# Kernel tuning notes

Measured on AMD Instinct MI355X. Metric: run time of the kernel, lower is better.

## Reference

```python
import jax, jax.numpy as jnp
import numpy as np

B, T, C = 4, 2048, 1024
H, D = 16, 64  # num_heads, head_size; H*D == C


def setup_inputs() -> dict:
    key = jax.random.key(0)
    k1, k2, k3 = jax.random.split(key, 3)
    x = jax.random.normal(k1, (B, T, C), dtype=jnp.float32)
    w_qkv = jax.random.normal(k2, (C, 3 * C), dtype=jnp.float32) * (C ** -0.5)
    w_out = jax.random.normal(k3, (C, C), dtype=jnp.float32) * (C ** -0.5)
    b_out = jnp.zeros((C,), dtype=jnp.float32)
    return {"x": x, "w_qkv": w_qkv, "w_out": w_out, "b_out": b_out}


def reference(x, w_qkv, w_out, b_out):
    Bb, Tt, Cc = x.shape
    qkv = x @ w_qkv                        # [B,T,3C]
    q, k, v = jnp.split(qkv, 3, axis=2)
    # [B,T,C] -> [B,H,T,D]
    q = q.reshape(Bb, Tt, H, D).transpose(0, 2, 1, 3)
    k = k.reshape(Bb, Tt, H, D).transpose(0, 2, 1, 3)
    v = v.reshape(Bb, Tt, H, D).transpose(0, 2, 1, 3)
    scores = jnp.einsum('bhqd,bhkd->bhqk', q, k) * (D ** -0.5)
    causal = jnp.tril(jnp.ones((Tt, Tt), dtype=bool))
    scores = jnp.where(causal, scores, -jnp.inf)
    attn = jax.nn.softmax(scores, axis=-1)  # dropout is identity in eval mode
    out = jnp.einsum('bhqk,bhkd->bhqd', attn, v)
    out = out.transpose(0, 2, 1, 3).reshape(Bb, Tt, Cc)
    return out @ w_out + b_out
```

## Files before the change

### kernel.cpp

```cpp
#include <hip/hip_runtime.h>

typedef __bf16 bf16;
typedef __bf16 bf16x4 __attribute__((ext_vector_type(4)));
typedef __bf16 bf16x8 __attribute__((ext_vector_type(8)));
typedef float  f32x4  __attribute__((ext_vector_type(4)));

#define MFMA16(A_, B_, C_) __builtin_amdgcn_mfma_f32_16x16x32_bf16((A_), (B_), (C_), 0, 0, 0)

#define BB 4
#define TT 2048
#define CC 1024
#define HH 16
#define DD 64
#define MM (BB * TT)
#define N_QKV (3 * CC)
#define LDSS 68
#define BSTRIDE 36
#define QSCALE 0.125f

static __device__ __forceinline__ void store_lds8(bf16* p, bf16x8 v) {
  bf16x4 lo, hi;
#pragma unroll
  for (int i = 0; i < 4; i++) { lo[i] = v[i]; hi[i] = v[i + 4]; }
  *(bf16x4*)p = lo;
  *(bf16x4*)(p + 4) = hi;
}

static __device__ __forceinline__ bf16x8 load_lds8(const bf16* p) {
  bf16x4 lo = *(const bf16x4*)p;
  bf16x4 hi = *(const bf16x4*)(p + 4);
  bf16x8 v;
#pragma unroll
  for (int i = 0; i < 4; i++) { v[i] = lo[i]; v[i + 4] = hi[i]; }
  return v;
}

__global__ __launch_bounds__(256) void sniff_k(const unsigned short* __restrict__ u,
                                               int* __restrict__ flag) {
  __shared__ int s;
  if (threadIdx.x == 0) s = 0;
  __syncthreads();
  int c = 0;
  for (int i = threadIdx.x; i < 65536; i += 256)
    if ((u[i] & 0x7F80u) == 0x7F80u) c = 1;
  if (c) atomicOr(&s, 1);
  __syncthreads();
  if (threadIdx.x == 0) *flag = s;
}

__global__ __launch_bounds__(256) void cvt_k(const void* __restrict__ in,
                                             bf16* __restrict__ out,
                                             const int* __restrict__ flag) {
  const int fl = *flag;
  const size_t i = ((size_t)blockIdx.x * 256 + threadIdx.x) * 8;
  if (fl) {
    f32x4 a = *(const f32x4*)((const float*)in + i);
    f32x4 b = *(const f32x4*)((const float*)in + i + 4);
    bf16x8 o;
#pragma unroll
    for (int j = 0; j < 4; j++) { o[j] = (bf16)a[j]; o[4 + j] = (bf16)b[j]; }
    *(bf16x8*)(out + i) = o;
  } else {
    *(bf16x8*)(out + i) = *(const bf16x8*)((const bf16*)in + i);
  }
}

__global__ __launch_bounds__(256) void transpose_k(const void* __restrict__ in,
                                                   bf16* __restrict__ out,
                                                   int R, int C,
                                                   const int* __restrict__ flag) {
  __shared__ bf16 tile[32][33];
  const int fl = *flag;
  const int c0 = blockIdx.x * 32, r0 = blockIdx.y * 32;
  const int tx = threadIdx.x & 31, ty = threadIdx.x >> 5;
#pragma unroll
  for (int i = ty; i < 32; i += 8) {
    const size_t idx = (size_t)(r0 + i) * C + c0 + tx;
    tile[i][tx] = fl ? (bf16)((const float*)in)[idx] : ((const bf16*)in)[idx];
  }
  __syncthreads();
#pragma unroll
  for (int i = ty; i < 32; i += 8)
    out[(size_t)(c0 + i) * R + r0 + tx] = tile[tx][i];
}

template <int EPI, bool AF>
__global__ __launch_bounds__(256) void gemm_bt(const void* __restrict__ Av,
                                               const bf16* __restrict__ Bt,
                                               const void* __restrict__ biasv,
                                               void* __restrict__ Cv,
                                               const int* __restrict__ flag,
                                               size_t aoff, size_t coff,
                                               int M, int N, int K,
                                               int lda, int ldc) {
  const int fl = *flag;
  const bool af32 = AF && (fl != 0);
  __shared__ __align__(16) bf16 sA[128 * 32];
  __shared__ __align__(16) bf16 sB[128 * 32];
  const int tid = threadIdx.x;
  const int lane = tid & 63, wave = tid >> 6;
  const int quad = lane >> 4, l15 = lane & 15;
  const int wr = wave >> 1, wc = wave & 1;
  const int m0 = blockIdx.x * 128, n0 = blockIdx.y * 128;
  const int srow = tid >> 2;
  const int scol = (tid & 3) * 8;

  f32x4 acc[4][4];
#pragma unroll
  for (int i = 0; i < 4; i++)
#pragma unroll
    for (int j = 0; j < 4; j++) {
      f32x4 z = {0.f, 0.f, 0.f, 0.f};
      acc[i][j] = z;
    }

  const size_t abase0 = aoff + (size_t)(m0 + srow) * lda + scol;
  const size_t abase1 = abase0 + (size_t)64 * lda;
  const bf16* Bg0 = Bt + (size_t)(n0 + srow) * K + scol;
  const bf16* Bg1 = Bg0 + (size_t)64 * K;

  for (int k0 = 0; k0 < K; k0 += 32) {
    bf16x8 a0, a1;
    if (af32) {
      const float* Af = (const float*)Av;
      f32x4 p00 = *(const f32x4*)(Af + abase0 + k0);
      f32x4 p01 = *(const f32x4*)(Af + abase0 + k0 + 4);
      f32x4 p10 = *(const f32x4*)(Af + abase1 + k0);
      f32x4 p11 = *(const f32x4*)(Af + abase1 + k0 + 4);
#pragma unroll
      for (int i = 0; i < 4; i++) {
        a0[i] = (bf16)p00[i]; a0[i + 4] = (bf16)p01[i];
        a1[i] = (bf16)p10[i]; a1[i + 4] = (bf16)p11[i];
      }
    } else {
      const bf16* Ab = (const bf16*)Av;
      a0 = *(const bf16x8*)(Ab + abase0 + k0);
      a1 = *(const bf16x8*)(Ab + abase1 + k0);
    }
    bf16x8 b0 = *(const bf16x8*)(Bg0 + k0);
    bf16x8 b1 = *(const bf16x8*)(Bg1 + k0);
    __syncthreads();
    *(bf16x8*)(sA + srow * 32 + scol) = a0;
    *(bf16x8*)(sA + (64 + srow) * 32 + scol) = a1;
    *(bf16x8*)(sB + srow * 32 + scol) = b0;
    *(bf16x8*)(sB + (64 + srow) * 32 + scol) = b1;
    __syncthreads();

    bf16x8 af[4], bfr[4];
#pragma unroll
    for (int mi = 0; mi < 4; mi++)
      af[mi] = *(const bf16x8*)(sA + (wr * 64 + mi * 16 + l15) * 32 + quad * 8);
#pragma unroll
    for (int ni = 0; ni < 4; ni++)
      bfr[ni] = *(const bf16x8*)(sB + (wc * 64 + ni * 16 + l15) * 32 + quad * 8);
#pragma unroll
    for (int mi = 0; mi < 4; mi++)
#pragma unroll
      for (int ni = 0; ni < 4; ni++)
        acc[mi][ni] = MFMA16(af[mi], bfr[ni], acc[mi][ni]);
  }

#pragma unroll
  for (int mi = 0; mi < 4; mi++) {
#pragma unroll
    for (int r = 0; r < 4; r++) {
      const int m = m0 + wr * 64 + mi * 16 + quad * 4 + r;
#pragma unroll
      for (int ni = 0; ni < 4; ni++) {
        const int n = n0 + wc * 64 + ni * 16 + l15;
        float v = acc[mi][ni][r];
        const size_t idx = coff + (size_t)m * ldc + n;
        if (EPI == 1) {
          v += fl ? ((const float*)biasv)[n] : (float)((const bf16*)biasv)[n];
          if (fl) ((float*)Cv)[idx] = v;
          else    ((bf16*)Cv)[idx] = (bf16)v;
        } else {
          ((bf16*)Cv)[idx] = (bf16)v;
        }
      }
    }
  }
}

template <int EPI, bool AF, bool WF>
__global__ __launch_bounds__(256) void gemm_nt(const void* __restrict__ Av,
                                               const void* __restrict__ Wv,
                                               const void* __restrict__ biasv,
                                               void* __restrict__ Cv,
                                               const int* __restrict__ flag,
                                               size_t aoff, size_t coff,
                                               int M, int N, int K,
                                               int lda, int ldc) {
  const int fl = *flag;
  const bool af32 = AF && (fl != 0);
  const bool wf32 = WF && (fl != 0);
  __shared__ __align__(16) bf16 sA[128 * 32];
  __shared__ __align__(16) bf16 sB[128 * BSTRIDE];
  const int tid = threadIdx.x;
  const int lane = tid & 63, wave = tid >> 6;
  const int quad = lane >> 4, l15 = lane & 15;
  const int wr = wave >> 1, wc = wave & 1;
  const int m0 = blockIdx.x * 128, n0 = blockIdx.y * 128;
  const int arow = tid >> 2, acol = (tid & 3) * 8;
  const int wk = tid >> 3, wn = (tid & 7) * 16;

  f32x4 acc[4][4];
#pragma unroll
  for (int i = 0; i < 4; i++)
#pragma unroll
    for (int j = 0; j < 4; j++) {
      f32x4 z = {0.f, 0.f, 0.f, 0.f};
      acc[i][j] = z;
    }

  const size_t abase0 = aoff + (size_t)(m0 + arow) * lda + acol;
  const size_t abase1 = abase0 + (size_t)64 * lda;

  for (int k0 = 0; k0 < K; k0 += 32) {
    bf16x8 a0, a1;
    if (af32) {
      const float* Af = (const float*)Av;
      f32x4 p00 = *(const f32x4*)(Af + abase0 + k0);
      f32x4 p01 = *(const f32x4*)(Af + abase0 + k0 + 4);
      f32x4 p10 = *(const f32x4*)(Af + abase1 + k0);
      f32x4 p11 = *(const f32x4*)(Af + abase1 + k0 + 4);
#pragma unroll
      for (int i = 0; i < 4; i++) {
        a0[i] = (bf16)p00[i]; a0[i + 4] = (bf16)p01[i];
        a1[i] = (bf16)p10[i]; a1[i + 4] = (bf16)p11[i];
      }
    } else {
      const bf16* Ab = (const bf16*)Av;
      a0 = *(const bf16x8*)(Ab + abase0 + k0);
      a1 = *(const bf16x8*)(Ab + abase1 + k0);
    }
    bf16 wreg[16];
    const size_t wbase = (size_t)(k0 + wk) * N + n0 + wn;
    if (wf32) {
      const float* Wf = (const float*)Wv;
      f32x4 q0 = *(const f32x4*)(Wf + wbase);
      f32x4 q1 = *(const f32x4*)(Wf + wbase + 4);
      f32x4 q2 = *(const f32x4*)(Wf + wbase + 8);
      f32x4 q3 = *(const f32x4*)(Wf + wbase + 12);
#pragma unroll
      for (int i = 0; i < 4; i++) {
        wreg[i] = (bf16)q0[i];      wreg[4 + i] = (bf16)q1[i];
        wreg[8 + i] = (bf16)q2[i];  wreg[12 + i] = (bf16)q3[i];
      }
    } else {
      const bf16* Wb = (const bf16*)Wv;
      bf16x8 w0 = *(const bf16x8*)(Wb + wbase);
      bf16x8 w1 = *(const bf16x8*)(Wb + wbase + 8);
#pragma unroll
      for (int i = 0; i < 8; i++) { wreg[i] = w0[i]; wreg[8 + i] = w1[i]; }
    }
    __syncthreads();
    *(bf16x8*)(sA + arow * 32 + acol) = a0;
    *(bf16x8*)(sA + (64 + arow) * 32 + acol) = a1;
#pragma unroll
    for (int i = 0; i < 16; i++)
      sB[(wn + i) * BSTRIDE + wk] = wreg[i];
    __syncthreads();

    bf16x8 af[4], bfr[4];
#pragma unroll
    for (int mi = 0; mi < 4; mi++)
      af[mi] = *(const bf16x8*)(sA + (wr * 64 + mi * 16 + l15) * 32 + quad * 8);
#pragma unroll
    for (int ni = 0; ni < 4; ni++)
      bfr[ni] = load_lds8(sB + (wc * 64 + ni * 16 + l15) * BSTRIDE + quad * 8);
#pragma unroll
    for (int mi = 0; mi < 4; mi++)
#pragma unroll
      for (int ni = 0; ni < 4; ni++)
        acc[mi][ni] = MFMA16(af[mi], bfr[ni], acc[mi][ni]);
  }

#pragma unroll
  for (int mi = 0; mi < 4; mi++) {
#pragma unroll
    for (int r = 0; r < 4; r++) {
      const int m = m0 + wr * 64 + mi * 16 + quad * 4 + r;
#pragma unroll
      for (int ni = 0; ni < 4; ni++) {
        const int n = n0 + wc * 64 + ni * 16 + l15;
        float v = acc[mi][ni][r];
        const size_t idx = coff + (size_t)m * ldc + n;
        if (EPI == 1) {
          v += fl ? ((const float*)biasv)[n] : (float)((const bf16*)biasv)[n];
          if (fl) ((float*)Cv)[idx] = v;
          else    ((bf16*)Cv)[idx] = (bf16)v;
        } else {
          ((bf16*)Cv)[idx] = (bf16)v;
        }
      }
    }
  }
}

__global__ __launch_bounds__(256) void attn_k(bf16* __restrict__ qkv) {
  __shared__ __align__(16) bf16 sQ[128 * LDSS];
  __shared__ __align__(16) bf16 sK[64 * LDSS];
  __shared__ __align__(16) bf16 sVt[64 * LDSS];

  const int tid = threadIdx.x;
  const int lane = tid & 63, wave = tid >> 6;
  const int quad = lane >> 4, l15 = lane & 15;
  const int bh = blockIdx.y;
  bf16* base = qkv + (size_t)(bh >> 4) * TT * N_QKV + (bh & 15) * DD;
  const bf16* Qp = base;
  const bf16* Kp = base + CC;
  const bf16* Vp = base + 2 * CC;

  const int krow = tid >> 2;
  const int kcol = (tid & 3) * 16;
  const int vkey = tid & 31;
  const int vcol = (tid >> 5) * 8;

  bf16x8 ones;
  {
    const bf16 o = (l15 == 0) ? (bf16)1.0f : (bf16)0.0f;
#pragma unroll
    for (int i = 0; i < 8; i++) ones[i] = o;
  }

  for (int pass = 0; pass < 2; pass++) {
    const int qt = pass ? (15 - (int)blockIdx.x) : (int)blockIdx.x;
    const int q0 = qt * 128;
    __syncthreads();

#pragma unroll
    for (int p = 0; p < 2; p++) {
      const int r = p * 64 + krow;
      const bf16* src = Qp + (size_t)(q0 + r) * N_QKV + kcol;
      bf16x8 v0 = *(const bf16x8*)src;
      bf16x8 v1 = *(const bf16x8*)(src + 8);
#pragma unroll
      for (int i = 0; i < 8; i++) {
        v0[i] = (bf16)((float)v0[i] * QSCALE);
        v1[i] = (bf16)((float)v1[i] * QSCALE);
      }
      store_lds8(sQ + r * LDSS + kcol, v0);
      store_lds8(sQ + r * LDSS + kcol + 8, v1);
    }

    bf16x8 kr0, kr1, vr0, vr1;
    {
      const bf16* kp = Kp + (size_t)krow * N_QKV + kcol;
      kr0 = *(const bf16x8*)kp;
      kr1 = *(const bf16x8*)(kp + 8);
      vr0 = *(const bf16x8*)(Vp + (size_t)vkey * N_QKV + vcol);
      vr1 = *(const bf16x8*)(Vp + (size_t)(32 + vkey) * N_QKV + vcol);
    }
    __syncthreads();

    bf16x8 aq[2][2];
#pragma unroll
    for (int mi = 0; mi < 2; mi++) {
      const bf16* qp = sQ + (size_t)(wave * 32 + mi * 16 + l15) * LDSS + quad * 8;
      aq[mi][0] = load_lds8(qp);
      aq[mi][1] = load_lds8(qp + 32);
    }

    f32x4 Oacc[2][4];
    f32x4 lacc[2];
#pragma unroll
    for (int mi = 0; mi < 2; mi++) {
      f32x4 z = {0.f, 0.f, 0.f, 0.f};
      lacc[mi] = z;
#pragma unroll
      for (int nt = 0; nt < 4; nt++) Oacc[mi][nt] = z;
    }

    const int jmax = q0 + 64;
    const int wave_row0 = q0 + wave * 32;
    bf16* sP = sQ + (size_t)(wave * 32) * LDSS;

    for (int j0 = 0; j0 <= jmax; j0 += 64) {
      __syncthreads();
      store_lds8(sK + krow * LDSS + kcol, kr0);
      store_lds8(sK + krow * LDSS + kcol + 8, kr1);
#pragma unroll
      for (int i = 0; i < 8; i++) {
        sVt[(vcol + i) * LDSS + vkey] = vr0[i];
        sVt[(vcol + i) * LDSS + 32 + vkey] = vr1[i];
      }
      __syncthreads();

      if (j0 + 64 <= jmax) {
        const bf16* kp = Kp + (size_t)(j0 + 64 + krow) * N_QKV + kcol;
        kr0 = *(const bf16x8*)kp;
        kr1 = *(const bf16x8*)(kp + 8);
        vr0 = *(const bf16x8*)(Vp + (size_t)(j0 + 64 + vkey) * N_QKV + vcol);
        vr1 = *(const bf16x8*)(Vp + (size_t)(j0 + 96 + vkey) * N_QKV + vcol);
      }

      if (j0 <= wave_row0 + 31) {
        f32x4 S[2][4];
#pragma unroll
        for (int nt = 0; nt < 4; nt++) {
          const bf16* kp = sK + (size_t)(nt * 16 + l15) * LDSS + quad * 8;
          bf16x8 bk0 = load_lds8(kp);
          bf16x8 bk1 = load_lds8(kp + 32);
#pragma unroll
          for (int mi = 0; mi < 2; mi++) {
            f32x4 acc = {0.f, 0.f, 0.f, 0.f};
            acc = MFMA16(aq[mi][0], bk0, acc);
            acc = MFMA16(aq[mi][1], bk1, acc);
            S[mi][nt] = acc;
          }
        }

        const bool needmask = (j0 + 63 > wave_row0);
#pragma unroll
        for (int mi = 0; mi < 2; mi++)
#pragma unroll
          for (int nt = 0; nt < 4; nt++) {
            const int kc = j0 + nt * 16 + l15;
#pragma unroll
            for (int r = 0; r < 4; r++) {
              const float e = __expf(S[mi][nt][r]);
              const bool dead =
                  needmask && (kc > wave_row0 + mi * 16 + quad * 4 + r);
              const float pv = dead ? 0.f : e;
              sP[(size_t)(mi * 16 + quad * 4 + r) * LDSS + nt * 16 + l15] =
                  (bf16)pv;
            }
          }

        bf16x8 ap[2][2];
#pragma unroll
        for (int mi = 0; mi < 2; mi++) {
          const bf16* pp = sP + (size_t)(mi * 16 + l15) * LDSS + quad * 8;
          ap[mi][0] = load_lds8(pp);
          ap[mi][1] = load_lds8(pp + 32);
          lacc[mi] = MFMA16(ap[mi][0], ones, lacc[mi]);
          lacc[mi] = MFMA16(ap[mi][1], ones, lacc[mi]);
        }
#pragma unroll
        for (int nt = 0; nt < 4; nt++) {
          const bf16* vp = sVt + (size_t)(nt * 16 + l15) * LDSS + quad * 8;
          bf16x8 bv0 = load_lds8(vp);
          bf16x8 bv1 = load_lds8(vp + 32);
#pragma unroll
          for (int mi = 0; mi < 2; mi++) {
            Oacc[mi][nt] = MFMA16(ap[mi][0], bv0, Oacc[mi][nt]);
            Oacc[mi][nt] = MFMA16(ap[mi][1], bv1, Oacc[mi][nt]);
          }
        }
      }
    }

#pragma unroll
    for (int mi = 0; mi < 2; mi++)
#pragma unroll
      for (int r = 0; r < 4; r++) {
        const float lv = __shfl(lacc[mi][r], lane & 48, 64);
        const float invl = 1.0f / lv;
        const int t = q0 + wave * 32 + mi * 16 + quad * 4 + r;
#pragma unroll
        for (int nt = 0; nt < 4; nt++)
          base[(size_t)t * N_QKV + nt * 16 + l15] =
              (bf16)(Oacc[mi][nt][r] * invl);
      }
  }
}

extern "C" void kernel_launch(void* const* d_in, const int* in_sizes, int n_in,
                              void* d_out, int out_size, void* d_ws, size_t ws_size,
                              hipStream_t stream) {
  const void* x = d_in[0];
  const void* w_qkv = d_in[1];
  const void* w_out = d_in[2];
  const void* b_out = d_in[3];

  int* flag = (int*)d_ws;
  char* p = (char*)d_ws + 256;
  bf16* wqkvT = (bf16*)p;
  bf16* woutT = wqkvT + (size_t)N_QKV * CC;

  const size_t wT_bytes = ((size_t)N_QKV * CC + (size_t)CC * CC) * 2;
  const size_t xb_bytes = (size_t)MM * CC * 2;
  const size_t qkv_bytes = (size_t)MM * N_QKV * 2;
  const size_t need_Ap = 256 + wT_bytes + xb_bytes + qkv_bytes;
  const size_t need_A  = 256 + wT_bytes + qkv_bytes;
  const size_t need_B  = 256 + wT_bytes + (size_t)TT * N_QKV * 2;

  sniff_k<<<1, 256, 0, stream>>>((const unsigned short*)x, flag);

  if (ws_size >= need_Ap) {
    bf16* xb = woutT + (size_t)CC * CC;
    bf16* qkv = xb + (size_t)MM * CC;
    cvt_k<<<(MM * CC) / 2048, 256, 0, stream>>>(x, xb, flag);
    transpose_k<<<dim3(N_QKV / 32, CC / 32), 256, 0, stream>>>(w_qkv, wqkvT, CC, N_QKV, flag);
    transpose_k<<<dim3(CC / 32, CC / 32), 256, 0, stream>>>(w_out, woutT, CC, CC, flag);

    gemm_bt<0, false><<<dim3(MM / 128, N_QKV / 128), 256, 0, stream>>>(
        xb, wqkvT, nullptr, qkv, flag, 0, 0, MM, N_QKV, CC, CC, N_QKV);

    attn_k<<<dim3(8, BB * HH), 256, 0, stream>>>(qkv);

    gemm_bt<1, false><<<dim3(MM / 128, CC / 128), 256, 0, stream>>>(
        qkv, woutT, b_out, d_out, flag, 0, 0, MM, CC, CC, N_QKV, CC);
  } else if (ws_size >= need_A) {
    bf16* qkv = woutT + (size_t)CC * CC;
    transpose_k<<<dim3(N_QKV / 32, CC / 32), 256, 0, stream>>>(w_qkv, wqkvT, CC, N_QKV, flag);
    transpose_k<<<dim3(CC / 32, CC / 32), 256, 0, stream>>>(w_out, woutT, CC, CC, flag);

    gemm_bt<0, true><<<dim3(MM / 128, N_QKV / 128), 256, 0, stream>>>(
        x, wqkvT, nullptr, qkv, flag, 0, 0, MM, N_QKV, CC, CC, N_QKV);

    attn_k<<<dim3(8, BB * HH), 256, 0, stream>>>(qkv);

    gemm_bt<1, false><<<dim3(MM / 128, CC / 128), 256, 0, stream>>>(
        qkv, woutT, b_out, d_out, flag, 0, 0, MM, CC, CC, N_QKV, CC);
  } else if (ws_size >= need_B) {
    bf16* qkv = woutT + (size_t)CC * CC;
    transpose_k<<<dim3(N_QKV / 32, CC / 32), 256, 0, stream>>>(w_qkv, wqkvT, CC, N_QKV, flag);
    transpose_k<<<dim3(CC / 32, CC / 32), 256, 0, stream>>>(w_out, woutT, CC, CC, flag);
    for (int b = 0; b < BB; b++) {
      const size_t xoff = (size_t)b * TT * CC;
      gemm_bt<0, true><<<dim3(TT / 128, N_QKV / 128), 256, 0, stream>>>(
          x, wqkvT, nullptr, qkv, flag, xoff, 0, TT, N_QKV, CC, CC, N_QKV);
      attn_k<<<dim3(8, HH), 256, 0, stream>>>(qkv);
      gemm_bt<1, false><<<dim3(TT / 128, CC / 128), 256, 0, stream>>>(
          qkv, woutT, b_out, d_out, flag, 0, xoff, TT, CC, CC, N_QKV, CC);
    }
  } else {
    bf16* qkvb = (bf16*)p;
    for (int b = 0; b < BB; b++) {
      const size_t xoff = (size_t)b * TT * CC;
      gemm_nt<0, true, true><<<dim3(TT / 128, N_QKV / 128), 256, 0, stream>>>(
          x, w_qkv, nullptr, qkvb, flag, xoff, 0, TT, N_QKV, CC, CC, N_QKV);
      attn_k<<<dim3(8, HH), 256, 0, stream>>>(qkvb);
      gemm_nt<1, false, true><<<dim3(TT / 128, CC / 128), 256, 0, stream>>>(
          qkvb, w_out, b_out, d_out, flag, 0, xoff, TT, CC, CC, N_QKV, CC);
    }
  }
}
```

Measured before the change: 334.7 us.

## Add direct-to-LDS async-copy GEMM and switch attention softmax to exp2

```diff
diff --git a/kernel.cpp b/kernel.cpp
--- a/kernel.cpp
+++ b/kernel.cpp
@@ -16,7 +16,7 @@
 #define N_QKV (3 * CC)
 #define LDSS 68
 #define BSTRIDE 36
-#define QSCALE 0.125f
+#define QSCALE2 0.18033688f
 
 static __device__ __forceinline__ void store_lds8(bf16* p, bf16x8 v) {
   bf16x4 lo, hi;
@@ -33,6 +33,12 @@
 #pragma unroll
   for (int i = 0; i < 4; i++) { v[i] = lo[i]; v[i + 4] = hi[i]; }
   return v;
+}
+
+static __device__ __forceinline__ void async_cp16(const bf16* g, bf16* l) {
+  __builtin_amdgcn_global_load_lds(
+      (const __attribute__((address_space(1))) void*)g,
+      (__attribute__((address_space(3))) void*)l, 16, 0, 0);
 }
 
 __global__ __launch_bounds__(256) void sniff_k(const unsigned short* __restrict__ u,
@@ -82,6 +88,86 @@
 #pragma unroll
   for (int i = ty; i < 32; i += 8)
     out[(size_t)(c0 + i) * R + r0 + tx] = tile[tx][i];
+}
+
+template <int EPI>
+__global__ __launch_bounds__(256) void gemm_lds(const bf16* __restrict__ A,
+                                                const bf16* __restrict__ Bt,
+                                                const void* __restrict__ biasv,
+                                                void* __restrict__ Cv,
+                                                const int* __restrict__ flag,
+                                                size_t aoff, size_t coff,
+                                                int M, int N, int K,
+                                                int lda, int ldc) {
+  const int fl = *flag;
+  __shared__ __align__(16) bf16 sA[128 * 32];
+  __shared__ __align__(16) bf16 sB[128 * 32];
+  const int tid = threadIdx.x;
+  const int lane = tid & 63, wave = tid >> 6;
+  const int quad = lane >> 4, l15 = lane & 15;
+  const int wr = wave >> 1, wc = wave & 1;
+  const int m0 = blockIdx.x * 128, n0 = blockIdx.y * 128;
+  const int grow = lane >> 2;
+  const int gcol = (lane & 3) * 8;
+
+  f32x4 acc[4][4];
+#pragma unroll
+  for (int i = 0; i < 4; i++)
+#pragma unroll
+    for (int j = 0; j < 4; j++) {
+      f32x4 z = {0.f, 0.f, 0.f, 0.f};
+      acc[i][j] = z;
+    }
+
+  const bf16* Ag = A + aoff + (size_t)(m0 + wave * 32 + grow) * lda + gcol;
+  const bf16* Bg = Bt + (size_t)(n0 + wave * 32 + grow) * K + gcol;
+  bf16* sAw = sA + wave * 32 * 32;
+  bf16* sBw = sB + wave * 32 * 32;
+
+  for (int k0 = 0; k0 < K; k0 += 32) {
+    __syncthreads();
+    async_cp16(Ag, sAw);
+    async_cp16(Ag + (size_t)16 * lda, sAw + 16 * 32);
+    async_cp16(Bg, sBw);
+    async_cp16(Bg + (size_t)16 * K, sBw + 16 * 32);
+    Ag += 32;
+    Bg += 32;
+    __syncthreads();
+
+    bf16x8 af[4], bfr[4];
+#pragma unroll
+    for (int mi = 0; mi < 4; mi++)
+      af[mi] = *(const bf16x8*)(sA + (wr * 64 + mi * 16 + l15) * 32 + quad * 8);
+#pragma unroll
+    for (int ni = 0; ni < 4; ni++)
+      bfr[ni] = *(const bf16x8*)(sB + (wc * 64 + ni * 16 + l15) * 32 + quad * 8);
+#pragma unroll
+    for (int mi = 0; mi < 4; mi++)
+#pragma unroll
+      for (int ni = 0; ni < 4; ni++)
+        acc[mi][ni] = MFMA16(af[mi], bfr[ni], acc[mi][ni]);
+  }
+
+#pragma unroll
+  for (int mi = 0; mi < 4; mi++) {
+#pragma unroll
+    for (int r = 0; r < 4; r++) {
+      const int m = m0 + wr * 64 + mi * 16 + quad * 4 + r;
+#pragma unroll
+      for (int ni = 0; ni < 4; ni++) {
+        const int n = n0 + wc * 64 + ni * 16 + l15;
+        float v = acc[mi][ni][r];
+        const size_t idx = coff + (size_t)m * ldc + n;
+        if (EPI == 1) {
+          v += fl ? ((const float*)biasv)[n] : (float)((const bf16*)biasv)[n];
+          if (fl) ((float*)Cv)[idx] = v;
+          else    ((bf16*)Cv)[idx] = (bf16)v;
+        } else {
+          ((bf16*)Cv)[idx] = (bf16)v;
+        }
+      }
+    }
+  }
 }
 
 template <int EPI, bool AF>
@@ -337,8 +423,8 @@
       bf16x8 v1 = *(const bf16x8*)(src + 8);
 #pragma unroll
       for (int i = 0; i < 8; i++) {
-        v0[i] = (bf16)((float)v0[i] * QSCALE);
-        v1[i] = (bf16)((float)v1[i] * QSCALE);
+        v0[i] = (bf16)((float)v0[i] * QSCALE2);
+        v1[i] = (bf16)((float)v1[i] * QSCALE2);
       }
       store_lds8(sQ + r * LDSS + kcol, v0);
       store_lds8(sQ + r * LDSS + kcol + 8, v1);
@@ -411,22 +497,30 @@
           }
         }
 
-        const bool needmask = (j0 + 63 > wave_row0);
-#pragma unroll
-        for (int mi = 0; mi < 2; mi++)
-#pragma unroll
-          for (int nt = 0; nt < 4; nt++) {
-            const int kc = j0 + nt * 16 + l15;
-#pragma unroll
-            for (int r = 0; r < 4; r++) {
-              const float e = __expf(S[mi][nt][r]);
-              const bool dead =
-                  needmask && (kc > wave_row0 + mi * 16 + quad * 4 + r);
-              const float pv = dead ? 0.f : e;
-              sP[(size_t)(mi * 16 + quad * 4 + r) * LDSS + nt * 16 + l15] =
-                  (bf16)pv;
+        if (j0 + 63 > wave_row0) {
+#pragma unroll
+          for (int mi = 0; mi < 2; mi++)
+#pragma unroll
+            for (int nt = 0; nt < 4; nt++) {
+              const int kc = j0 + nt * 16 + l15;
+#pragma unroll
+              for (int r = 0; r < 4; r++) {
+                const float e = __builtin_amdgcn_exp2f(S[mi][nt][r]);
+                const bool dead = kc > wave_row0 + mi * 16 + quad * 4 + r;
+                sP[(size_t)(mi * 16 + quad * 4 + r) * LDSS + nt * 16 + l15] =
+                    (bf16)(dead ? 0.f : e);
+              }
             }
-          }
+        } else {
+#pragma unroll
+          for (int mi = 0; mi < 2; mi++)
+#pragma unroll
+            for (int nt = 0; nt < 4; nt++)
+#pragma unroll
+              for (int r = 0; r < 4; r++)
+                sP[(size_t)(mi * 16 + quad * 4 + r) * LDSS + nt * 16 + l15] =
+                    (bf16)__builtin_amdgcn_exp2f(S[mi][nt][r]);
+        }
 
         bf16x8 ap[2][2];
 #pragma unroll
@@ -495,12 +589,12 @@
     transpose_k<<<dim3(N_QKV / 32, CC / 32), 256, 0, stream>>>(w_qkv, wqkvT, CC, N_QKV, flag);
     transpose_k<<<dim3(CC / 32, CC / 32), 256, 0, stream>>>(w_out, woutT, CC, CC, flag);
 
-    gemm_bt<0, false><<<dim3(MM / 128, N_QKV / 128), 256, 0, stream>>>(
+    gemm_lds<0><<<dim3(MM / 128, N_QKV / 128), 256, 0, stream>>>(
         xb, wqkvT, nullptr, qkv, flag, 0, 0, MM, N_QKV, CC, CC, N_QKV);
 
     attn_k<<<dim3(8, BB * HH), 256, 0, stream>>>(qkv);
 
-    gemm_bt<1, false><<<dim3(MM / 128, CC / 128), 256, 0, stream>>>(
+    gemm_lds<1><<<dim3(MM / 128, CC / 128), 256, 0, stream>>>(
         qkv, woutT, b_out, d_out, flag, 0, 0, MM, CC, CC, N_QKV, CC);
   } else if (ws_size >= need_A) {
     bf16* qkv = woutT + (size_t)CC * CC;
@@ -512,7 +606,7 @@
 
     attn_k<<<dim3(8, BB * HH), 256, 0, stream>>>(qkv);
 
-    gemm_bt<1, false><<<dim3(MM / 128, CC / 128), 256, 0, stream>>>(
+    gemm_lds<1><<<dim3(MM / 128, CC / 128), 256, 0, stream>>>(
         qkv, woutT, b_out, d_out, flag, 0, 0, MM, CC, CC, N_QKV, CC);
   } else if (ws_size >= need_B) {
     bf16* qkv = woutT + (size_t)CC * CC;
@@ -523,7 +617,7 @@
       gemm_bt<0, true><<<dim3(TT / 128, N_QKV / 128), 256, 0, stream>>>(
           x, wqkvT, nullptr, qkv, flag, xoff, 0, TT, N_QKV, CC, CC, N_QKV);
       attn_k<<<dim3(8, HH), 256, 0, stream>>>(qkv);
-      gemm_bt<1, false><<<dim3(TT / 128, CC / 128), 256, 0, stream>>>(
+      gemm_lds<1><<<dim3(TT / 128, CC / 128), 256, 0, stream>>>(
           qkv, woutT, b_out, d_out, flag, 0, xoff, TT, CC, CC, N_QKV, CC);
     }
   } else {
```

Measured after the change: 332.6 us. About the same (-0.6%).
